# Kernel tuning notes

Measured on AMD Instinct MI355X. Metric: run time of the kernel, lower is better.

Reference implementation:

```python
import jax, jax.numpy as jnp
import numpy as np

WS = 7        # window_size
HEADS = 3
HEAD_DIM = 32


def _relative_indices(ws):
    idx = np.array([[x, y] for x in range(ws) for y in range(ws)])  # [ws*ws, 2]
    dist = idx[None, :, :] - idx[:, None, :]
    dist[:, :, 0] += ws - 1
    dist[:, :, 1] += ws - 1
    dist[:, :, 0] *= 2 * ws - 1
    return jnp.asarray(dist.sum(-1))  # [ws*ws, ws*ws] int


_REL_IDX = _relative_indices(WS)


def setup_inputs() -> dict:
    key = jax.random.key(0)
    k1, k2, k3, k4, k5 = jax.random.split(key, 5)
    dim = 96
    inner = HEADS * HEAD_DIM  # 96
    return {
        "x": jax.random.normal(k1, (64, dim, 56, 56), dtype=jnp.float32),
        "w_qkv": jax.random.normal(k2, (dim, inner * 3), dtype=jnp.float32) * 0.05,
        "pos_emb": jax.random.normal(k3, ((2 * WS - 1) ** 2, HEADS), dtype=jnp.float32),
        "w_out": jax.random.normal(k4, (inner, dim), dtype=jnp.float32) * 0.05,
        "b_out": jax.random.normal(k5, (dim,), dtype=jnp.float32),
    }


def _to_windows(t, b, H, W, ws, h, d):
    # [b, H, W, h*d] -> [b, h, nw_h*nw_w, ws*ws, d]  (non-shuffle layout)
    nwh, nww = H // ws, W // ws
    t = t.reshape(b, nwh, ws, nww, ws, h, d)
    t = t.transpose(0, 5, 1, 3, 2, 4, 6)  # b h nwh nww wh ww d
    return t.reshape(b, h, nwh * nww, ws * ws, d)


def reference(x, w_qkv, pos_emb, w_out, b_out):
    ws, h, d = WS, HEADS, HEAD_DIM
    scale = d ** (-0.5)
    x = x.transpose(0, 2, 3, 1)  # b, H, W, c
    b, H, W, _ = x.shape
    nwh, nww = H // ws, W // ws
    qkv = x @ w_qkv  # b, H, W, 3*inner
    q, k, v = jnp.split(qkv, 3, axis=-1)
    q = _to_windows(q, b, H, W, ws, h, d)
    k = _to_windows(k, b, H, W, ws, h, d)
    v = _to_windows(v, b, H, W, ws, h, d)
    dots = jnp.einsum('bhwid,bhwjd->bhwij', q, k) * scale
    # relative position bias: gather [ws*ws, ws*ws, heads] -> [1, h, 1, i, j]
    bias = pos_emb[_REL_IDX]  # [ws*ws, ws*ws, h]
    dots = dots + bias.transpose(2, 0, 1)[None, :, None]
    attn = jax.nn.softmax(dots, axis=-1)
    out = jnp.einsum('bhwij,bhwjd->bhwid', attn, v)  # b h nw ws*ws d
    out = out.reshape(b, h, nwh, nww, ws, ws, d)
    out = out.transpose(0, 2, 4, 3, 5, 1, 6).reshape(b, H, W, h * d)
    out = out @ w_out + b_out
    return out.transpose(0, 3, 1, 2)  # b, dim, H, W
```

## Files before the change

kernel.cpp:

```cpp
#include <hip/hip_runtime.h>

typedef __bf16 bf16;
typedef __bf16 bf16x4 __attribute__((ext_vector_type(4)));
typedef __bf16 bf16x8 __attribute__((ext_vector_type(8)));
typedef float  f32x4  __attribute__((ext_vector_type(4)));

#define SCALE 0.17677669529663687f

#define XWIN_OFF  0
#define WQKVT_OFF 50331648
#define WOUTT_OFF 50386944
#define BIASC_OFF 50405376

#define CBAR() asm volatile("" ::: "memory")

template <int CTRL>
__device__ __forceinline__ float dpp_mv(float x) {
    return __int_as_float(__builtin_amdgcn_update_dpp(
        0, __float_as_int(x), CTRL, 0xF, 0xF, true));
}
__device__ __forceinline__ float row16_max(float m) {
    m = fmaxf(m, dpp_mv<0xB1>(m));
    m = fmaxf(m, dpp_mv<0x4E>(m));
    m = fmaxf(m, dpp_mv<0x124>(m));
    m = fmaxf(m, dpp_mv<0x128>(m));
    return m;
}
__device__ __forceinline__ float row16_sum(float s) {
    s += dpp_mv<0xB1>(s);
    s += dpp_mv<0x4E>(s);
    s += dpp_mv<0x124>(s);
    s += dpp_mv<0x128>(s);
    return s;
}

__global__ __launch_bounds__(512)
void pre(const float* __restrict__ x, const float* __restrict__ wqkv,
         const float* __restrict__ pos, const float* __restrict__ wout,
         bf16* __restrict__ xwin, bf16* __restrict__ wqkvT,
         bf16* __restrict__ woutT, float* __restrict__ biasC)
{
    __shared__ bf16 xs[392 * 50];
    if (blockIdx.x < 512) {
        const int tid = threadIdx.x;
        const int b = blockIdx.x >> 3, wh = blockIdx.x & 7;
        const float* xb = x + (size_t)b * 96 * 3136 + wh * 7 * 56;
        bf16* xo = xwin + ((size_t)b * 64 + wh * 8) * 64 * 96;
        for (int c0 = 0; c0 < 96; c0 += 48) {
            if (c0) __syncthreads();
            for (int i = tid; i < 48 * 392; i += 512) {
                int c = i / 392, t = i - c * 392;
                xs[t * 50 + c] = (bf16)xb[(size_t)(c0 + c) * 3136 + t];
            }
            __syncthreads();
            for (int i = tid; i < 8 * 64 * 48; i += 512) {
                int c = i % 48;
                int wt = (i / 48) & 63;
                int win = i / (48 * 64);
                bf16 v = (bf16)0.f;
                if (wt < 49) v = xs[((wt / 7) * 56 + win * 7 + (wt % 7)) * 50 + c];
                xo[(win * 64 + wt) * 96 + c0 + c] = v;
            }
        }
    } else {
        int tid = (blockIdx.x - 512) * 512 + threadIdx.x;
        const int stride = 4 * 512;
        for (int i = tid; i < 288 * 96; i += stride) {
            int n = i / 96, c = i % 96;
            float v = wqkv[c * 288 + n];
            if (n < 96) v *= SCALE;
            wqkvT[i] = (bf16)v;
        }
        for (int i = tid; i < 96 * 96; i += stride) {
            int o = i / 96, c = i % 96;
            woutT[i] = (bf16)wout[c * 96 + o];
        }
        for (int i = tid; i < 3 * 4 * 4 * 64 * 4; i += stride) {
            int e = i & 3, lane = (i >> 2) & 63, wv = (i >> 8) & 3, ni = (i >> 10) & 3, h = i >> 12;
            int row = wv * 16 + ((lane >> 4) << 2) + e;
            int col = ni * 16 + (lane & 15);
            float v;
            if (col >= 49) v = -1e30f;
            else if (row >= 49) v = 0.f;
            else {
                int ridx = ((col / 7) - (row / 7) + 6) * 13 + ((col % 7) - (row % 7) + 6);
                v = pos[ridx * 3 + h];
            }
            biasC[i] = v;
        }
    }
}

__global__ __launch_bounds__(256, 4)
void winattn(const bf16* __restrict__ xwin, const float* __restrict__ bout,
             const bf16* __restrict__ wqkvT, const bf16* __restrict__ woutT,
             const float* __restrict__ biasC, float* __restrict__ out)
{
    __shared__ __align__(16) unsigned char smem[40448];
    bf16* qall = (bf16*)(smem);
    bf16* kall = (bf16*)(smem + 13312);
    bf16* vt   = (bf16*)(smem + 26624);
    bf16* Ost  = (bf16*)(smem);
    float* fin = (float*)(smem + 13312);

    const int tid = threadIdx.x;
    const int w = tid >> 6, lane = tid & 63;
    const int lr = lane & 15, lk = lane >> 4;

    const int blkraw = blockIdx.x;
    const int b  = blkraw >> 6;
    const int wh = blkraw & 7;
    const int ww = (blkraw >> 3) & 7;
    const int win = wh * 8 + ww;
    const int row0 = wh * 7, col0 = ww * 7;
    const bf16* xg = xwin + (size_t)(b * 64 + win) * 64 * 96;

    {
        bf16x8 a[4][3];
#pragma unroll
        for (int mi = 0; mi < 4; ++mi)
#pragma unroll
            for (int k = 0; k < 3; ++k)
                a[mi][k] = *(const bf16x8*)&xg[(mi * 16 + lr) * 96 + k * 32 + lk * 8];
        const int ni0  = (w < 2) ? w * 5 : 10 + (w - 2) * 4;
        const int ncnt = (w < 2) ? 5 : 4;
#pragma unroll
        for (int j = 0; j < 5; ++j) {
            if (j < ncnt) {
                const int ni = ni0 + j;
                f32x4 acc[4];
#pragma unroll
                for (int mi = 0; mi < 4; ++mi) acc[mi] = (f32x4){0.f, 0.f, 0.f, 0.f};
#pragma unroll
                for (int k = 0; k < 3; ++k) {
                    bf16x8 bb = *(const bf16x8*)&wqkvT[(ni * 16 + lr) * 96 + k * 32 + lk * 8];
#pragma unroll
                    for (int mi = 0; mi < 4; ++mi)
                        acc[mi] = __builtin_amdgcn_mfma_f32_16x16x32_bf16(a[mi][k], bb, acc[mi], 0, 0, 0);
                }
                if (ni < 6) {
#pragma unroll
                    for (int mi = 0; mi < 4; ++mi)
#pragma unroll
                        for (int e = 0; e < 4; ++e)
                            qall[(mi * 16 + lk * 4 + e) * 104 + ni * 16 + lr] = (bf16)acc[mi][e];
                } else if (ni < 12) {
#pragma unroll
                    for (int mi = 0; mi < 4; ++mi)
#pragma unroll
                        for (int e = 0; e < 4; ++e)
                            kall[(mi * 16 + lk * 4 + e) * 104 + (ni - 6) * 16 + lr] = (bf16)acc[mi][e];
                } else {
#pragma unroll
                    for (int mi = 0; mi < 4; ++mi) {
                        bf16x4 pk;
#pragma unroll
                        for (int e = 0; e < 4; ++e) pk[e] = (bf16)acc[mi][e];
                        *(bf16x4*)&vt[((ni - 12) * 16 + lr) * 72 + mi * 16 + lk * 4] = pk;
                    }
                }
            }
        }
    }
    f32x4 bias0[4], bias1[4], bias2[4];
#pragma unroll
    for (int ni = 0; ni < 4; ++ni)
        bias0[ni] = *(const f32x4*)&biasC[(size_t)((0 * 4 + ni) * 4 + w) * 256 + lane * 4];
    __syncthreads();

    bf16x8 qa[3];
#pragma unroll
    for (int h = 0; h < 3; ++h)
        qa[h] = *(const bf16x8*)&qall[(w * 16 + lr) * 104 + h * 32 + lk * 8];
    CBAR();

    bf16* Pw = (bf16*)(smem + w * 3328);

    f32x4 oacc[3][2];
    float inv[3][4];
#pragma unroll
    for (int h = 0; h < 3; ++h)
#pragma unroll
        for (int ni = 0; ni < 2; ++ni) oacc[h][ni] = (f32x4){0.f, 0.f, 0.f, 0.f};

#pragma unroll
    for (int h = 0; h < 3; ++h) {
        f32x4 sacc[4];
        const f32x4* bc = (h == 0) ? bias0 : (h == 1) ? bias1 : bias2;
#pragma unroll
        for (int ni = 0; ni < 4; ++ni) {
            bf16x8 kb = *(const bf16x8*)&kall[(ni * 16 + lr) * 104 + h * 32 + lk * 8];
            sacc[ni] = __builtin_amdgcn_mfma_f32_16x16x32_bf16(qa[h], kb, bc[ni], 0, 0, 0);
        }
        if (h == 0) {
#pragma unroll
            for (int ni = 0; ni < 4; ++ni)
                bias1[ni] = *(const f32x4*)&biasC[(size_t)((1 * 4 + ni) * 4 + w) * 256 + lane * 4];
        } else if (h == 1) {
#pragma unroll
            for (int ni = 0; ni < 4; ++ni)
                bias2[ni] = *(const f32x4*)&biasC[(size_t)((2 * 4 + ni) * 4 + w) * 256 + lane * 4];
        }
#pragma unroll
        for (int e = 0; e < 4; ++e) {
            float s0 = sacc[0][e], s1 = sacc[1][e], s2 = sacc[2][e], s3 = sacc[3][e];
            float m = row16_max(fmaxf(fmaxf(s0, s1), fmaxf(s2, s3)));
            float p0 = __expf(s0 - m), p1 = __expf(s1 - m);
            float p2 = __expf(s2 - m), p3 = __expf(s3 - m);
            float s = row16_sum((p0 + p1) + (p2 + p3));
            inv[h][e] = __builtin_amdgcn_rcpf(s);
            int rl = lk * 4 + e;
            Pw[rl * 72 + lr]      = (bf16)p0;
            Pw[rl * 72 + 16 + lr] = (bf16)p1;
            Pw[rl * 72 + 32 + lr] = (bf16)p2;
            Pw[rl * 72 + 48 + lr] = (bf16)p3;
        }
        CBAR();
#pragma unroll
        for (int kk = 0; kk < 2; ++kk) {
            bf16x8 pa = *(const bf16x8*)&Pw[lr * 72 + kk * 32 + lk * 8];
#pragma unroll
            for (int ni = 0; ni < 2; ++ni) {
                bf16x8 vb = *(const bf16x8*)&vt[(h * 32 + ni * 16 + lr) * 72 + kk * 32 + lk * 8];
                oacc[h][ni] = __builtin_amdgcn_mfma_f32_16x16x32_bf16(pa, vb, oacc[h][ni], 0, 0, 0);
            }
        }
        CBAR();
    }

#pragma unroll
    for (int h = 0; h < 3; ++h)
#pragma unroll
        for (int ni = 0; ni < 2; ++ni)
#pragma unroll
            for (int e = 0; e < 4; ++e)
                Ost[(w * 16 + lk * 4 + e) * 104 + h * 32 + ni * 16 + lr]
                    = (bf16)(oacc[h][ni][e] * inv[h][e]);
    __syncthreads();

    {
        const int pcnt = (w < 2) ? 2 : 1;
#pragma unroll
        for (int j = 0; j < 2; ++j) {
            if (j < pcnt) {
                const int ni = w + j * 4;
                const float bo = bout[ni * 16 + lr];
                f32x4 pacc[4];
#pragma unroll
                for (int mi = 0; mi < 4; ++mi) pacc[mi] = (f32x4){0.f, 0.f, 0.f, 0.f};
#pragma unroll
                for (int k = 0; k < 3; ++k) {
                    bf16x8 wb = *(const bf16x8*)&woutT[(ni * 16 + lr) * 96 + k * 32 + lk * 8];
#pragma unroll
                    for (int mi = 0; mi < 4; ++mi) {
                        bf16x8 as = *(const bf16x8*)&Ost[(mi * 16 + lr) * 104 + k * 32 + lk * 8];
                        pacc[mi] = __builtin_amdgcn_mfma_f32_16x16x32_bf16(as, wb, pacc[mi], 0, 0, 0);
                    }
                }
#pragma unroll
                for (int mi = 0; mi < 4; ++mi)
#pragma unroll
                    for (int e = 0; e < 4; ++e)
                        fin[(mi * 16 + lk * 4 + e) * 101 + ni * 16 + lr] = pacc[mi][e] + bo;
            }
        }
    }
    __syncthreads();

    {
        const int t = lane;
        if (t < 49) {
            const int off = (row0 + t / 7) * 56 + col0 + t % 7;
            float* ob = out + (size_t)(b * 96 + w * 24) * 3136 + off;
            const float* fr = fin + t * 101 + w * 24;
#pragma unroll
            for (int j = 0; j < 24; ++j)
                ob[(size_t)j * 3136] = fr[j];
        }
    }
}

extern "C" void kernel_launch(void* const* d_in, const int* in_sizes, int n_in,
                              void* d_out, int out_size, void* d_ws, size_t ws_size,
                              hipStream_t stream) {
    const float* x    = (const float*)d_in[0];
    const float* wqkv = (const float*)d_in[1];
    const float* pos  = (const float*)d_in[2];
    const float* wout = (const float*)d_in[3];
    const float* bout = (const float*)d_in[4];
    float* outp = (float*)d_out;

    bf16*  xwin  = (bf16*)((char*)d_ws + XWIN_OFF);
    bf16*  wqkvT = (bf16*)((char*)d_ws + WQKVT_OFF);
    bf16*  woutT = (bf16*)((char*)d_ws + WOUTT_OFF);
    float* biasC = (float*)((char*)d_ws + BIASC_OFF);

    pre<<<dim3(516), dim3(512), 0, stream>>>(x, wqkv, pos, wout,
                                             xwin, wqkvT, woutT, biasC);
    winattn<<<dim3(4096), dim3(256), 0, stream>>>(xwin, bout, wqkvT, woutT,
                                                  biasC, outp);
}
```

Baseline: 97.14 us.

## Swap MFMA operand order to vectorize LDS stores and rebalance out-projection

Swaps the A/B operands of the QKV, PV and output-projection MFMAs so each lane's accumulator holds consecutive columns. This lets Q, K, O and the final output tile be written to shared memory as packed bf16x4/float4 stores instead of scalar ones. The softmax normalization is applied to P before the PV product rather than to O afterwards. The output projection work is split evenly into 6 tiles per wave instead of an uneven 2/1 split. The fin row stride changes from 101 to 104 to allow aligned float4 stores, which may add bank conflicts on the final strided read.

```diff
diff --git a/kernel.cpp b/kernel.cpp
--- a/kernel.cpp
+++ b/kernel.cpp
@@ -116,12 +116,12 @@
     const bf16* xg = xwin + (size_t)(b * 64 + win) * 64 * 96;
 
     {
-        bf16x8 a[4][3];
-#pragma unroll
-        for (int mi = 0; mi < 4; ++mi)
+        bf16x8 xb[4][3];
+#pragma unroll
+        for (int mt = 0; mt < 4; ++mt)
 #pragma unroll
             for (int k = 0; k < 3; ++k)
-                a[mi][k] = *(const bf16x8*)&xg[(mi * 16 + lr) * 96 + k * 32 + lk * 8];
+                xb[mt][k] = *(const bf16x8*)&xg[(mt * 16 + lr) * 96 + k * 32 + lk * 8];
         const int ni0  = (w < 2) ? w * 5 : 10 + (w - 2) * 4;
         const int ncnt = (w < 2) ? 5 : 4;
 #pragma unroll
@@ -130,34 +130,36 @@
                 const int ni = ni0 + j;
                 f32x4 acc[4];
 #pragma unroll
-                for (int mi = 0; mi < 4; ++mi) acc[mi] = (f32x4){0.f, 0.f, 0.f, 0.f};
+                for (int mt = 0; mt < 4; ++mt) acc[mt] = (f32x4){0.f, 0.f, 0.f, 0.f};
 #pragma unroll
                 for (int k = 0; k < 3; ++k) {
-                    bf16x8 bb = *(const bf16x8*)&wqkvT[(ni * 16 + lr) * 96 + k * 32 + lk * 8];
-#pragma unroll
-                    for (int mi = 0; mi < 4; ++mi)
-                        acc[mi] = __builtin_amdgcn_mfma_f32_16x16x32_bf16(a[mi][k], bb, acc[mi], 0, 0, 0);
+                    bf16x8 wa = *(const bf16x8*)&wqkvT[(ni * 16 + lr) * 96 + k * 32 + lk * 8];
+#pragma unroll
+                    for (int mt = 0; mt < 4; ++mt)
+                        acc[mt] = __builtin_amdgcn_mfma_f32_16x16x32_bf16(wa, xb[mt][k], acc[mt], 0, 0, 0);
                 }
                 if (ni < 6) {
 #pragma unroll
-                    for (int mi = 0; mi < 4; ++mi)
+                    for (int mt = 0; mt < 4; ++mt) {
+                        bf16x4 pk;
+#pragma unroll
+                        for (int e = 0; e < 4; ++e) pk[e] = (bf16)acc[mt][e];
+                        *(bf16x4*)&qall[(mt * 16 + lr) * 104 + ni * 16 + lk * 4] = pk;
+                    }
+                } else if (ni < 12) {
+#pragma unroll
+                    for (int mt = 0; mt < 4; ++mt) {
+                        bf16x4 pk;
+#pragma unroll
+                        for (int e = 0; e < 4; ++e) pk[e] = (bf16)acc[mt][e];
+                        *(bf16x4*)&kall[(mt * 16 + lr) * 104 + (ni - 6) * 16 + lk * 4] = pk;
+                    }
+                } else {
+#pragma unroll
+                    for (int mt = 0; mt < 4; ++mt)
 #pragma unroll
                         for (int e = 0; e < 4; ++e)
-                            qall[(mi * 16 + lk * 4 + e) * 104 + ni * 16 + lr] = (bf16)acc[mi][e];
-                } else if (ni < 12) {
-#pragma unroll
-                    for (int mi = 0; mi < 4; ++mi)
-#pragma unroll
-                        for (int e = 0; e < 4; ++e)
-                            kall[(mi * 16 + lk * 4 + e) * 104 + (ni - 6) * 16 + lr] = (bf16)acc[mi][e];
-                } else {
-#pragma unroll
-                    for (int mi = 0; mi < 4; ++mi) {
-                        bf16x4 pk;
-#pragma unroll
-                        for (int e = 0; e < 4; ++e) pk[e] = (bf16)acc[mi][e];
-                        *(bf16x4*)&vt[((ni - 12) * 16 + lr) * 72 + mi * 16 + lk * 4] = pk;
-                    }
+                            vt[((ni - 12) * 16 + lk * 4 + e) * 72 + mt * 16 + lr] = (bf16)acc[mt][e];
                 }
             }
         }
@@ -177,11 +179,10 @@
     bf16* Pw = (bf16*)(smem + w * 3328);
 
     f32x4 oacc[3][2];
-    float inv[3][4];
 #pragma unroll
     for (int h = 0; h < 3; ++h)
 #pragma unroll
-        for (int ni = 0; ni < 2; ++ni) oacc[h][ni] = (f32x4){0.f, 0.f, 0.f, 0.f};
+        for (int dt = 0; dt < 2; ++dt) oacc[h][dt] = (f32x4){0.f, 0.f, 0.f, 0.f};
 
 #pragma unroll
     for (int h = 0; h < 3; ++h) {
@@ -208,21 +209,21 @@
             float p0 = __expf(s0 - m), p1 = __expf(s1 - m);
             float p2 = __expf(s2 - m), p3 = __expf(s3 - m);
             float s = row16_sum((p0 + p1) + (p2 + p3));
-            inv[h][e] = __builtin_amdgcn_rcpf(s);
+            float inv = __builtin_amdgcn_rcpf(s);
             int rl = lk * 4 + e;
-            Pw[rl * 72 + lr]      = (bf16)p0;
-            Pw[rl * 72 + 16 + lr] = (bf16)p1;
-            Pw[rl * 72 + 32 + lr] = (bf16)p2;
-            Pw[rl * 72 + 48 + lr] = (bf16)p3;
+            Pw[rl * 72 + lr]      = (bf16)(p0 * inv);
+            Pw[rl * 72 + 16 + lr] = (bf16)(p1 * inv);
+            Pw[rl * 72 + 32 + lr] = (bf16)(p2 * inv);
+            Pw[rl * 72 + 48 + lr] = (bf16)(p3 * inv);
         }
         CBAR();
 #pragma unroll
         for (int kk = 0; kk < 2; ++kk) {
             bf16x8 pa = *(const bf16x8*)&Pw[lr * 72 + kk * 32 + lk * 8];
 #pragma unroll
-            for (int ni = 0; ni < 2; ++ni) {
-                bf16x8 vb = *(const bf16x8*)&vt[(h * 32 + ni * 16 + lr) * 72 + kk * 32 + lk * 8];
-                oacc[h][ni] = __builtin_amdgcn_mfma_f32_16x16x32_bf16(pa, vb, oacc[h][ni], 0, 0, 0);
+            for (int dt = 0; dt < 2; ++dt) {
+                bf16x8 vb = *(const bf16x8*)&vt[(h * 32 + dt * 16 + lr) * 72 + kk * 32 + lk * 8];
+                oacc[h][dt] = __builtin_amdgcn_mfma_f32_16x16x32_bf16(vb, pa, oacc[h][dt], 0, 0, 0);
             }
         }
         CBAR();
@@ -231,38 +232,31 @@
 #pragma unroll
     for (int h = 0; h < 3; ++h)
 #pragma unroll
-        for (int ni = 0; ni < 2; ++ni)
-#pragma unroll
-            for (int e = 0; e < 4; ++e)
-                Ost[(w * 16 + lk * 4 + e) * 104 + h * 32 + ni * 16 + lr]
-                    = (bf16)(oacc[h][ni][e] * inv[h][e]);
+        for (int dt = 0; dt < 2; ++dt) {
+            bf16x4 pk;
+#pragma unroll
+            for (int e = 0; e < 4; ++e) pk[e] = (bf16)oacc[h][dt][e];
+            *(bf16x4*)&Ost[(w * 16 + lr) * 104 + h * 32 + dt * 16 + lk * 4] = pk;
+        }
     __syncthreads();
 
     {
-        const int pcnt = (w < 2) ? 2 : 1;
-#pragma unroll
-        for (int j = 0; j < 2; ++j) {
-            if (j < pcnt) {
-                const int ni = w + j * 4;
-                const float bo = bout[ni * 16 + lr];
-                f32x4 pacc[4];
-#pragma unroll
-                for (int mi = 0; mi < 4; ++mi) pacc[mi] = (f32x4){0.f, 0.f, 0.f, 0.f};
-#pragma unroll
-                for (int k = 0; k < 3; ++k) {
-                    bf16x8 wb = *(const bf16x8*)&woutT[(ni * 16 + lr) * 96 + k * 32 + lk * 8];
-#pragma unroll
-                    for (int mi = 0; mi < 4; ++mi) {
-                        bf16x8 as = *(const bf16x8*)&Ost[(mi * 16 + lr) * 104 + k * 32 + lk * 8];
-                        pacc[mi] = __builtin_amdgcn_mfma_f32_16x16x32_bf16(as, wb, pacc[mi], 0, 0, 0);
-                    }
-                }
-#pragma unroll
-                for (int mi = 0; mi < 4; ++mi)
-#pragma unroll
-                    for (int e = 0; e < 4; ++e)
-                        fin[(mi * 16 + lk * 4 + e) * 101 + ni * 16 + lr] = pacc[mi][e] + bo;
-            }
+#pragma unroll
+        for (int j = 0; j < 6; ++j) {
+            const int p  = w * 6 + j;
+            const int ni = p >> 2, mt = p & 3;
+            f32x4 pacc = (f32x4){0.f, 0.f, 0.f, 0.f};
+#pragma unroll
+            for (int k = 0; k < 3; ++k) {
+                bf16x8 wa = *(const bf16x8*)&woutT[(ni * 16 + lr) * 96 + k * 32 + lk * 8];
+                bf16x8 ob = *(const bf16x8*)&Ost[(mt * 16 + lr) * 104 + k * 32 + lk * 8];
+                pacc = __builtin_amdgcn_mfma_f32_16x16x32_bf16(wa, ob, pacc, 0, 0, 0);
+            }
+            float4 bo4 = *(const float4*)&bout[ni * 16 + lk * 4];
+            float4 f;
+            f.x = pacc[0] + bo4.x; f.y = pacc[1] + bo4.y;
+            f.z = pacc[2] + bo4.z; f.w = pacc[3] + bo4.w;
+            *(float4*)&fin[(mt * 16 + lr) * 104 + ni * 16 + lk * 4] = f;
         }
     }
     __syncthreads();
@@ -272,7 +266,7 @@
         if (t < 49) {
             const int off = (row0 + t / 7) * 56 + col0 + t % 7;
             float* ob = out + (size_t)(b * 96 + w * 24) * 3136 + off;
-            const float* fr = fin + t * 101 + w * 24;
+            const float* fr = fin + t * 104 + w * 24;
 #pragma unroll
             for (int j = 0; j < 24; ++j)
                 ob[(size_t)j * 3136] = fr[j];
```

Result: slower. 102.7 us (+5.7%).

## Fuse input windowing into attention kernel, drop bf16 xwin intermediate

Applied to the files above, without the earlier changes.

The pre-pass that transposed x into a windowed bf16 buffer in global memory is removed. Each attention block now reads its 7x7 window straight from the fp32 NCHW input and converts it into shared memory. The QKV projection work is rebalanced across waves, with V results held in registers until after a barrier, and softmax normalisation is folded into P before the PV MFMA. This avoids a full global write and re-read of the input, at the cost of strided, poorly coalesced fp32 loads inside the attention kernel and an extra block barrier.

```diff
diff --git a/kernel.cpp b/kernel.cpp
--- a/kernel.cpp
+++ b/kernel.cpp
@@ -7,10 +7,9 @@
 
 #define SCALE 0.17677669529663687f
 
-#define XWIN_OFF  0
-#define WQKVT_OFF 50331648
-#define WOUTT_OFF 50386944
-#define BIASC_OFF 50405376
+#define WQKVT_OFF 0
+#define WOUTT_OFF 55296
+#define BIASC_OFF 73728
 
 #define CBAR() asm volatile("" ::: "memory")
 
@@ -35,64 +34,39 @@
 }
 
 __global__ __launch_bounds__(512)
-void pre(const float* __restrict__ x, const float* __restrict__ wqkv,
-         const float* __restrict__ pos, const float* __restrict__ wout,
-         bf16* __restrict__ xwin, bf16* __restrict__ wqkvT,
-         bf16* __restrict__ woutT, float* __restrict__ biasC)
+void prep(const float* __restrict__ wqkv, const float* __restrict__ pos,
+          const float* __restrict__ wout, bf16* __restrict__ wqkvT,
+          bf16* __restrict__ woutT, float* __restrict__ biasC)
 {
-    __shared__ bf16 xs[392 * 50];
-    if (blockIdx.x < 512) {
-        const int tid = threadIdx.x;
-        const int b = blockIdx.x >> 3, wh = blockIdx.x & 7;
-        const float* xb = x + (size_t)b * 96 * 3136 + wh * 7 * 56;
-        bf16* xo = xwin + ((size_t)b * 64 + wh * 8) * 64 * 96;
-        for (int c0 = 0; c0 < 96; c0 += 48) {
-            if (c0) __syncthreads();
-            for (int i = tid; i < 48 * 392; i += 512) {
-                int c = i / 392, t = i - c * 392;
-                xs[t * 50 + c] = (bf16)xb[(size_t)(c0 + c) * 3136 + t];
-            }
-            __syncthreads();
-            for (int i = tid; i < 8 * 64 * 48; i += 512) {
-                int c = i % 48;
-                int wt = (i / 48) & 63;
-                int win = i / (48 * 64);
-                bf16 v = (bf16)0.f;
-                if (wt < 49) v = xs[((wt / 7) * 56 + win * 7 + (wt % 7)) * 50 + c];
-                xo[(win * 64 + wt) * 96 + c0 + c] = v;
-            }
-        }
-    } else {
-        int tid = (blockIdx.x - 512) * 512 + threadIdx.x;
-        const int stride = 4 * 512;
-        for (int i = tid; i < 288 * 96; i += stride) {
-            int n = i / 96, c = i % 96;
-            float v = wqkv[c * 288 + n];
-            if (n < 96) v *= SCALE;
-            wqkvT[i] = (bf16)v;
-        }
-        for (int i = tid; i < 96 * 96; i += stride) {
-            int o = i / 96, c = i % 96;
-            woutT[i] = (bf16)wout[c * 96 + o];
-        }
-        for (int i = tid; i < 3 * 4 * 4 * 64 * 4; i += stride) {
-            int e = i & 3, lane = (i >> 2) & 63, wv = (i >> 8) & 3, ni = (i >> 10) & 3, h = i >> 12;
-            int row = wv * 16 + ((lane >> 4) << 2) + e;
-            int col = ni * 16 + (lane & 15);
-            float v;
-            if (col >= 49) v = -1e30f;
-            else if (row >= 49) v = 0.f;
-            else {
-                int ridx = ((col / 7) - (row / 7) + 6) * 13 + ((col % 7) - (row % 7) + 6);
-                v = pos[ridx * 3 + h];
-            }
-            biasC[i] = v;
-        }
+    int tid = blockIdx.x * 512 + threadIdx.x;
+    const int stride = 4 * 512;
+    for (int i = tid; i < 288 * 96; i += stride) {
+        int n = i / 96, c = i % 96;
+        float v = wqkv[c * 288 + n];
+        if (n < 96) v *= SCALE;
+        wqkvT[i] = (bf16)v;
+    }
+    for (int i = tid; i < 96 * 96; i += stride) {
+        int o = i / 96, c = i % 96;
+        woutT[i] = (bf16)wout[c * 96 + o];
+    }
+    for (int i = tid; i < 3 * 4 * 4 * 64 * 4; i += stride) {
+        int e = i & 3, lane = (i >> 2) & 63, wv = (i >> 8) & 3, ni = (i >> 10) & 3, h = i >> 12;
+        int row = wv * 16 + ((lane >> 4) << 2) + e;
+        int col = ni * 16 + (lane & 15);
+        float v;
+        if (col >= 49) v = -1e30f;
+        else if (row >= 49) v = 0.f;
+        else {
+            int ridx = ((col / 7) - (row / 7) + 6) * 13 + ((col % 7) - (row % 7) + 6);
+            v = pos[ridx * 3 + h];
+        }
+        biasC[i] = v;
     }
 }
 
 __global__ __launch_bounds__(256, 4)
-void winattn(const bf16* __restrict__ xwin, const float* __restrict__ bout,
+void winattn(const float* __restrict__ x, const float* __restrict__ bout,
              const bf16* __restrict__ wqkvT, const bf16* __restrict__ woutT,
              const float* __restrict__ biasC, float* __restrict__ out)
 {
@@ -100,6 +74,7 @@
     bf16* qall = (bf16*)(smem);
     bf16* kall = (bf16*)(smem + 13312);
     bf16* vt   = (bf16*)(smem + 26624);
+    bf16* xs   = (bf16*)(smem + 26624);
     bf16* Ost  = (bf16*)(smem);
     float* fin = (float*)(smem + 13312);
 
@@ -111,56 +86,70 @@
     const int b  = blkraw >> 6;
     const int wh = blkraw & 7;
     const int ww = (blkraw >> 3) & 7;
-    const int win = wh * 8 + ww;
     const int row0 = wh * 7, col0 = ww * 7;
-    const bf16* xg = xwin + (size_t)(b * 64 + win) * 64 * 96;
-
+
+    {
+        const int t = lane;
+        const int c0 = (tid >> 6) * 24;
+        const bool valid = t < 49;
+        const int tr = valid ? t / 7 : 0, tc = valid ? t % 7 : 0;
+        const float* xp = x + ((size_t)(b * 96 + c0)) * 3136
+                            + (row0 + tr) * 56 + col0 + tc;
+        bf16* xw = &xs[t * 108 + c0];
+#pragma unroll
+        for (int j = 0; j < 24; ++j) {
+            float v = xp[(size_t)j * 3136];
+            xw[j] = (bf16)(valid ? v : 0.f);
+        }
+    }
+    __syncthreads();
+
+    f32x4 vh0[4], vh1[4];
     {
         bf16x8 a[4][3];
 #pragma unroll
         for (int mi = 0; mi < 4; ++mi)
 #pragma unroll
-            for (int k = 0; k < 3; ++k)
-                a[mi][k] = *(const bf16x8*)&xg[(mi * 16 + lr) * 96 + k * 32 + lk * 8];
-        const int ni0  = (w < 2) ? w * 5 : 10 + (w - 2) * 4;
-        const int ncnt = (w < 2) ? 5 : 4;
-#pragma unroll
-        for (int j = 0; j < 5; ++j) {
-            if (j < ncnt) {
-                const int ni = ni0 + j;
-                f32x4 acc[4];
-#pragma unroll
-                for (int mi = 0; mi < 4; ++mi) acc[mi] = (f32x4){0.f, 0.f, 0.f, 0.f};
-#pragma unroll
-                for (int k = 0; k < 3; ++k) {
-                    bf16x8 bb = *(const bf16x8*)&wqkvT[(ni * 16 + lr) * 96 + k * 32 + lk * 8];
-#pragma unroll
-                    for (int mi = 0; mi < 4; ++mi)
-                        acc[mi] = __builtin_amdgcn_mfma_f32_16x16x32_bf16(a[mi][k], bb, acc[mi], 0, 0, 0);
-                }
-                if (ni < 6) {
-#pragma unroll
-                    for (int mi = 0; mi < 4; ++mi)
-#pragma unroll
-                        for (int e = 0; e < 4; ++e)
-                            qall[(mi * 16 + lk * 4 + e) * 104 + ni * 16 + lr] = (bf16)acc[mi][e];
-                } else if (ni < 12) {
-#pragma unroll
-                    for (int mi = 0; mi < 4; ++mi)
-#pragma unroll
-                        for (int e = 0; e < 4; ++e)
-                            kall[(mi * 16 + lk * 4 + e) * 104 + (ni - 6) * 16 + lr] = (bf16)acc[mi][e];
-                } else {
-#pragma unroll
-                    for (int mi = 0; mi < 4; ++mi) {
-                        bf16x4 pk;
-#pragma unroll
-                        for (int e = 0; e < 4; ++e) pk[e] = (bf16)acc[mi][e];
-                        *(bf16x4*)&vt[((ni - 12) * 16 + lr) * 72 + mi * 16 + lk * 4] = pk;
-                    }
-                }
-            }
-        }
+            for (int k = 0; k < 3; ++k) {
+                bf16x4 lo = *(const bf16x4*)&xs[(mi * 16 + lr) * 108 + k * 32 + lk * 8];
+                bf16x4 hi = *(const bf16x4*)&xs[(mi * 16 + lr) * 108 + k * 32 + lk * 8 + 4];
+                a[mi][k] = __builtin_shufflevector(lo, hi, 0, 1, 2, 3, 4, 5, 6, 7);
+            }
+        CBAR();
+
+        auto compute = [&](int ni, f32x4 (&acc)[4]) {
+#pragma unroll
+            for (int mi = 0; mi < 4; ++mi) acc[mi] = (f32x4){0.f, 0.f, 0.f, 0.f};
+#pragma unroll
+            for (int k = 0; k < 3; ++k) {
+                bf16x8 bb = *(const bf16x8*)&wqkvT[(ni * 16 + lr) * 96 + k * 32 + lk * 8];
+#pragma unroll
+                for (int mi = 0; mi < 4; ++mi)
+                    acc[mi] = __builtin_amdgcn_mfma_f32_16x16x32_bf16(a[mi][k], bb, acc[mi], 0, 0, 0);
+            }
+        };
+        auto writeQ = [&](int ni, f32x4 (&acc)[4]) {
+#pragma unroll
+            for (int mi = 0; mi < 4; ++mi)
+#pragma unroll
+                for (int e = 0; e < 4; ++e)
+                    qall[(mi * 16 + lk * 4 + e) * 104 + ni * 16 + lr] = (bf16)acc[mi][e];
+        };
+        auto writeK = [&](int ni, f32x4 (&acc)[4]) {
+#pragma unroll
+            for (int mi = 0; mi < 4; ++mi)
+#pragma unroll
+                for (int e = 0; e < 4; ++e)
+                    kall[(mi * 16 + lk * 4 + e) * 104 + (ni - 6) * 16 + lr] = (bf16)acc[mi][e];
+        };
+
+        f32x4 acc[4];
+        compute(w, acc);          writeQ(w, acc);
+        compute(w + 4, acc);
+        if (w < 2) writeQ(w + 4, acc); else writeK(w + 4, acc);
+        compute(w + 8, acc);      writeK(w + 8, acc);
+        compute(w + 12, vh0);
+        if (w < 2) compute(w + 16, vh1);
     }
     f32x4 bias0[4], bias1[4], bias2[4];
 #pragma unroll
@@ -168,16 +157,33 @@
         bias0[ni] = *(const f32x4*)&biasC[(size_t)((0 * 4 + ni) * 4 + w) * 256 + lane * 4];
     __syncthreads();
 
+    {
+#pragma unroll
+        for (int mi = 0; mi < 4; ++mi) {
+            bf16x4 pk;
+#pragma unroll
+            for (int e = 0; e < 4; ++e) pk[e] = (bf16)vh0[mi][e];
+            *(bf16x4*)&vt[((w + 12 - 12) * 16 + lr) * 72 + mi * 16 + lk * 4] = pk;
+        }
+        if (w < 2) {
+#pragma unroll
+            for (int mi = 0; mi < 4; ++mi) {
+                bf16x4 pk;
+#pragma unroll
+                for (int e = 0; e < 4; ++e) pk[e] = (bf16)vh1[mi][e];
+                *(bf16x4*)&vt[((w + 16 - 12) * 16 + lr) * 72 + mi * 16 + lk * 4] = pk;
+            }
+        }
+    }
     bf16x8 qa[3];
 #pragma unroll
     for (int h = 0; h < 3; ++h)
         qa[h] = *(const bf16x8*)&qall[(w * 16 + lr) * 104 + h * 32 + lk * 8];
-    CBAR();
+    __syncthreads();
 
     bf16* Pw = (bf16*)(smem + w * 3328);
 
     f32x4 oacc[3][2];
-    float inv[3][4];
 #pragma unroll
     for (int h = 0; h < 3; ++h)
 #pragma unroll
@@ -208,12 +214,12 @@
             float p0 = __expf(s0 - m), p1 = __expf(s1 - m);
             float p2 = __expf(s2 - m), p3 = __expf(s3 - m);
             float s = row16_sum((p0 + p1) + (p2 + p3));
-            inv[h][e] = __builtin_amdgcn_rcpf(s);
+            float inv = __builtin_amdgcn_rcpf(s);
             int rl = lk * 4 + e;
-            Pw[rl * 72 + lr]      = (bf16)p0;
-            Pw[rl * 72 + 16 + lr] = (bf16)p1;
-            Pw[rl * 72 + 32 + lr] = (bf16)p2;
-            Pw[rl * 72 + 48 + lr] = (bf16)p3;
+            Pw[rl * 72 + lr]      = (bf16)(p0 * inv);
+            Pw[rl * 72 + 16 + lr] = (bf16)(p1 * inv);
+            Pw[rl * 72 + 32 + lr] = (bf16)(p2 * inv);
+            Pw[rl * 72 + 48 + lr] = (bf16)(p3 * inv);
         }
         CBAR();
 #pragma unroll
@@ -235,7 +241,7 @@
 #pragma unroll
             for (int e = 0; e < 4; ++e)
                 Ost[(w * 16 + lk * 4 + e) * 104 + h * 32 + ni * 16 + lr]
-                    = (bf16)(oacc[h][ni][e] * inv[h][e]);
+                    = (bf16)oacc[h][ni][e];
     __syncthreads();
 
     {
@@ -290,13 +296,11 @@
     const float* bout = (const float*)d_in[4];
     float* outp = (float*)d_out;
 
-    bf16*  xwin  = (bf16*)((char*)d_ws + XWIN_OFF);
     bf16*  wqkvT = (bf16*)((char*)d_ws + WQKVT_OFF);
     bf16*  woutT = (bf16*)((char*)d_ws + WOUTT_OFF);
     float* biasC = (float*)((char*)d_ws + BIASC_OFF);
 
-    pre<<<dim3(516), dim3(512), 0, stream>>>(x, wqkv, pos, wout,
-                                             xwin, wqkvT, woutT, biasC);
-    winattn<<<dim3(4096), dim3(256), 0, stream>>>(xwin, bout, wqkvT, woutT,
+    prep<<<dim3(4), dim3(512), 0, stream>>>(wqkv, pos, wout, wqkvT, woutT, biasC);
+    winattn<<<dim3(4096), dim3(256), 0, stream>>>(x, bout, wqkvT, woutT,
                                                   biasC, outp);
 }
```

Result: faster. 80.83 us (median of 2 runs) (-16.8%).
